# Kernel tuning notes

Measured on AMD Instinct MI355X. Metric: run time of the kernel, lower is better.

The kernel has to match this reference:

```python
import jax, jax.numpy as jnp
import numpy as np

DIM = 1024
HEADS = 16
D_HEAD = 64
INNER = HEADS * D_HEAD  # 1024
CTX_DIM = 768
FF_INNER = 4 * DIM  # 4096
EPS = 1e-5
SCALE = D_HEAD ** -0.5


def _layer_norm(x, g, b):
    m = jnp.mean(x, axis=-1, keepdims=True)
    v = jnp.mean(jnp.square(x - m), axis=-1, keepdims=True)
    return (x - m) * jax.lax.rsqrt(v + EPS) * g + b


def _attention(x, ctx, wq, wk, wv, wo, bo):
    B, S, _ = x.shape
    T = ctx.shape[1]
    # project and split heads -> [B, H, S, Dh]
    q = (x @ wq).reshape(B, S, HEADS, D_HEAD).transpose(0, 2, 1, 3)
    k = (ctx @ wk).reshape(B, T, HEADS, D_HEAD).transpose(0, 2, 1, 3)
    v = (ctx @ wv).reshape(B, T, HEADS, D_HEAD).transpose(0, 2, 1, 3)
    attn = jnp.einsum('bhid,bhjd->bhij', q, k) * SCALE
    attn = jax.nn.softmax(attn, axis=-1)
    out = jnp.einsum('bhij,bhjd->bhid', attn, v)  # [B, H, S, Dh]
    out = out.transpose(0, 2, 1, 3).reshape(B, S, INNER)
    return out @ wo + bo


def setup_inputs() -> dict:
    key = jax.random.key(0)
    ks = jax.random.split(key, 20)
    rn = lambda k, shape, s=0.02: jax.random.normal(k, shape, dtype=jnp.float32) * s
    inp = {
        'hidden_states': jax.random.normal(ks[0], (4, 2048, DIM), dtype=jnp.float32),
        'context': jax.random.normal(ks[1], (4, 77, CTX_DIM), dtype=jnp.float32),
        # self-attention
        'wq1': rn(ks[2], (DIM, INNER)), 'wk1': rn(ks[3], (DIM, INNER)),
        'wv1': rn(ks[4], (DIM, INNER)),
        'wo1': rn(ks[5], (INNER, DIM)), 'bo1': jnp.zeros((DIM,), jnp.float32),
        # cross-attention (k/v from context dim 768)
        'wq2': rn(ks[6], (DIM, INNER)), 'wk2': rn(ks[7], (CTX_DIM, INNER)),
        'wv2': rn(ks[8], (CTX_DIM, INNER)),
        'wo2': rn(ks[9], (INNER, DIM)), 'bo2': jnp.zeros((DIM,), jnp.float32),
        # GEGLU feed-forward
        'w_ff1': rn(ks[10], (DIM, 2 * FF_INNER)), 'b_ff1': jnp.zeros((2 * FF_INNER,), jnp.float32),
        'w_ff2': rn(ks[11], (FF_INNER, DIM)), 'b_ff2': jnp.zeros((DIM,), jnp.float32),
        # layer norms
        'ln1_g': jnp.ones((DIM,), jnp.float32), 'ln1_b': jnp.zeros((DIM,), jnp.float32),
        'ln2_g': jnp.ones((DIM,), jnp.float32), 'ln2_b': jnp.zeros((DIM,), jnp.float32),
        'ln3_g': jnp.ones((DIM,), jnp.float32), 'ln3_b': jnp.zeros((DIM,), jnp.float32),
    }
    return inp


def reference(hidden_states, context, wq1, wk1, wv1, wo1, bo1,
              wq2, wk2, wv2, wo2, bo2, w_ff1, b_ff1, w_ff2, b_ff2,
              ln1_g, ln1_b, ln2_g, ln2_b, ln3_g, ln3_b):
    # self-attention, pre-norm residual
    h = hidden_states
    h = h + _attention(_layer_norm(h, ln1_g, ln1_b), _layer_norm(h, ln1_g, ln1_b),
                       wq1, wk1, wv1, wo1, bo1)
    # cross-attention
    h = h + _attention(_layer_norm(h, ln2_g, ln2_b), context,
                       wq2, wk2, wv2, wo2, bo2)
    # GEGLU feed-forward
    x = _layer_norm(h, ln3_g, ln3_b) @ w_ff1 + b_ff1
    lin, gate = jnp.split(x, 2, axis=2)
    h = h + (lin * jax.nn.gelu(gate)) @ w_ff2 + b_ff2
    return h
```

## Files before the change

kernel.cpp:

```cpp
#include <hip/hip_runtime.h>

#define DIMM 1024
#define NHEADS 16
#define DHEAD 64
#define BATCH 4
#define SEQ 2048
#define TCTX 77
#define CTXD 768
#define FFI 4096

typedef float f32x4 __attribute__((ext_vector_type(4)));
typedef __bf16 bf16x8 __attribute__((ext_vector_type(8)));

__device__ __forceinline__ float bf2f(unsigned short u){
  union { unsigned int i; float f; } c; c.i = ((unsigned int)u) << 16; return c.f;
}
__device__ __forceinline__ unsigned short f2bf(float f){
  union { float f; unsigned int i; } c; c.f = f;
  unsigned int i = c.i;
  return (unsigned short)((i + 0x7fffu + ((i >> 16) & 1u)) >> 16);
}
__device__ __forceinline__ unsigned short f2bf_fast(float f){
  union { float f; unsigned int i; } c; c.f = f;
  return (unsigned short)((c.i + 0x8000u) >> 16);
}
__device__ __forceinline__ void cp16(const unsigned short* g, unsigned short* l){
  __builtin_amdgcn_global_load_lds(
      (const __attribute__((address_space(1))) unsigned int*)g,
      (__attribute__((address_space(3))) unsigned int*)l, 16, 0, 0);
}

__global__ __launch_bounds__(256) void ln_kernel(const float* __restrict__ x,
                                                 const float* __restrict__ g,
                                                 const float* __restrict__ bb,
                                                 unsigned short* __restrict__ y)
{
  int row = blockIdx.x, tid = threadIdx.x;
  float4 raw = ((const float4*)(x + (size_t)row * DIMM))[tid];
  float v0 = raw.x, v1 = raw.y, v2 = raw.z, v3 = raw.w;
  float s  = v0 + v1 + v2 + v3;
  float sq = v0*v0 + v1*v1 + v2*v2 + v3*v3;
  #pragma unroll
  for (int off = 32; off; off >>= 1){ s += __shfl_xor(s, off); sq += __shfl_xor(sq, off); }
  __shared__ float sm[8];
  int wave = tid >> 6, lane = tid & 63;
  if (lane == 0){ sm[wave] = s; sm[4 + wave] = sq; }
  __syncthreads();
  s  = sm[0] + sm[1] + sm[2] + sm[3];
  sq = sm[4] + sm[5] + sm[6] + sm[7];
  float mean = s * (1.f / DIMM);
  float var  = sq * (1.f / DIMM) - mean * mean;
  float rstd = rsqrtf(var + 1e-5f);
  float4 gr = ((const float4*)g)[tid];
  float4 br = ((const float4*)bb)[tid];
  ushort4 o;
  o.x = f2bf((v0 - mean) * rstd * gr.x + br.x);
  o.y = f2bf((v1 - mean) * rstd * gr.y + br.y);
  o.z = f2bf((v2 - mean) * rstd * gr.z + br.z);
  o.w = f2bf((v3 - mean) * rstd * gr.w + br.w);
  ((ushort4*)(y + (size_t)row * DIMM))[tid] = o;
}

__global__ __launch_bounds__(256) void wt_kernel(const float* __restrict__ in,
                                                 unsigned short* __restrict__ out,
                                                 int K, int N)
{
  __shared__ float t[32][33];
  int tx = threadIdx.x & 31, ty = threadIdx.x >> 5;
  int k0 = blockIdx.y * 32, n0 = blockIdx.x * 32;
  #pragma unroll
  for (int i = 0; i < 4; i++)
    t[ty + i * 8][tx] = in[(size_t)(k0 + ty + i * 8) * N + n0 + tx];
  __syncthreads();
  #pragma unroll
  for (int i = 0; i < 4; i++)
    out[(size_t)(n0 + ty + i * 8) * K + k0 + tx] = f2bf(t[tx][ty + i * 8]);
}

#define CTXE (TCTX * BATCH * CTXD)
__global__ __launch_bounds__(256) void ctxcvt_kernel(const float* __restrict__ in,
                                                     unsigned short* __restrict__ out)
{
  int e = (blockIdx.x * 256 + threadIdx.x) * 4;
  float4 v;
  if (e < CTXE) v = *(const float4*)(in + e);
  else { v.x = 0.f; v.y = 0.f; v.z = 0.f; v.w = 0.f; }
  ushort4 o; o.x = f2bf(v.x); o.y = f2bf(v.y); o.z = f2bf(v.z); o.w = f2bf(v.w);
  *(ushort4*)(out + e) = o;
}

template<int RESF, int CF32>
__global__ __launch_bounds__(256) void gemm_bt(
    const unsigned short* __restrict__ A, int lda,
    const unsigned short* __restrict__ Bt, int ldb,
    const float* __restrict__ bias, const void* __restrict__ resv,
    void* __restrict__ Cv, int ldc,
    int M, int N, int K)
{
  __shared__ __align__(16) unsigned short As[128][64];
  __shared__ __align__(16) unsigned short Bs[128][64];
  int tid = threadIdx.x;
  int n0 = blockIdx.x * 128, row0 = blockIdx.y * 128;
  int wave = tid >> 6, lane = tid & 63, quad = lane >> 4, l16 = lane & 15;
  int wm = (wave >> 1) * 64, wn = (wave & 1) * 64;
  int wrow = wave * 32;
  int lrow = lane >> 3, lgrp = lane & 7;
  int gcol = ((lgrp ^ lrow) * 8);

  f32x4 acc[4][4];
  #pragma unroll
  for (int mt = 0; mt < 4; mt++)
    #pragma unroll
    for (int nt = 0; nt < 4; nt++) acc[mt][nt] = 0.f;

  for (int k0 = 0; k0 < K; k0 += 64) {
    const unsigned short* ga = A  + (size_t)(row0 + wrow + lrow) * lda + k0 + gcol;
    const unsigned short* gb = Bt + (size_t)(n0  + wrow + lrow) * ldb + k0 + gcol;
    #pragma unroll
    for (int i = 0; i < 4; i++){
      cp16(ga + (size_t)(8 * i) * lda, &As[wrow + 8 * i][0]);
      cp16(gb + (size_t)(8 * i) * ldb, &Bs[wrow + 8 * i][0]);
    }
    __syncthreads();
    #pragma unroll
    for (int kc = 0; kc < 2; kc++){
      bf16x8 af[4], bf[4];
      #pragma unroll
      for (int mt = 0; mt < 4; mt++){
        int R = wm + mt * 16 + l16;
        af[mt] = *(const bf16x8*)&As[R][((kc * 4 + quad) ^ (R & 7)) * 8];
      }
      #pragma unroll
      for (int nt = 0; nt < 4; nt++){
        int R = wn + nt * 16 + l16;
        bf[nt] = *(const bf16x8*)&Bs[R][((kc * 4 + quad) ^ (R & 7)) * 8];
      }
      #pragma unroll
      for (int mt = 0; mt < 4; mt++)
        #pragma unroll
        for (int nt = 0; nt < 4; nt++)
          acc[mt][nt] = __builtin_amdgcn_mfma_f32_16x16x32_bf16(af[mt], bf[nt], acc[mt][nt], 0, 0, 0);
    }
    __syncthreads();
  }

  #pragma unroll
  for (int nt = 0; nt < 4; nt++){
    int c = n0 + wn + nt * 16 + l16;
    float bv = bias ? bias[c] : 0.f;
    #pragma unroll
    for (int mt = 0; mt < 4; mt++){
      int rbase = row0 + wm + mt * 16 + quad * 4;
      #pragma unroll
      for (int rr = 0; rr < 4; rr++){
        int r = rbase + rr;
        if (r < M) {
          float val = acc[mt][nt][rr] + bv;
          size_t idx = (size_t)r * ldc + c;
          if (RESF) val += ((const float*)resv)[idx];
          if (CF32) ((float*)Cv)[idx] = val;
          else      ((unsigned short*)Cv)[idx] = f2bf(val);
        }
      }
    }
  }
}

__global__ __launch_bounds__(256) void ff1_geglu_bt(
    const unsigned short* __restrict__ A,
    const unsigned short* __restrict__ BtW,
    const float* __restrict__ bias,
    unsigned short* __restrict__ Z, int M)
{
  __shared__ __align__(16) unsigned short As[128][64];
  __shared__ __align__(16) unsigned short BsL[128][64];
  __shared__ __align__(16) unsigned short BsG[128][64];
  int tid = threadIdx.x;
  int n0 = blockIdx.x * 128, row0 = blockIdx.y * 128;
  int wave = tid >> 6, lane = tid & 63, quad = lane >> 4, l16 = lane & 15;
  int wm = (wave >> 1) * 64, wn = (wave & 1) * 64;
  int wrow = wave * 32;
  int lrow = lane >> 3, lgrp = lane & 7;
  int gcol = ((lgrp ^ lrow) * 8);

  f32x4 accL[4][4], accG[4][4];
  #pragma unroll
  for (int mt = 0; mt < 4; mt++)
    #pragma unroll
    for (int nt = 0; nt < 4; nt++){ accL[mt][nt] = 0.f; accG[mt][nt] = 0.f; }

  for (int k0 = 0; k0 < DIMM; k0 += 64) {
    const unsigned short* ga = A   + (size_t)(row0 + wrow + lrow) * DIMM + k0 + gcol;
    const unsigned short* gl = BtW + (size_t)(n0  + wrow + lrow) * DIMM + k0 + gcol;
    const unsigned short* gg = BtW + (size_t)(FFI + n0 + wrow + lrow) * DIMM + k0 + gcol;
    #pragma unroll
    for (int i = 0; i < 4; i++){
      cp16(ga + (size_t)(8 * i) * DIMM, &As[wrow + 8 * i][0]);
      cp16(gl + (size_t)(8 * i) * DIMM, &BsL[wrow + 8 * i][0]);
      cp16(gg + (size_t)(8 * i) * DIMM, &BsG[wrow + 8 * i][0]);
    }
    __syncthreads();
    #pragma unroll
    for (int kc = 0; kc < 2; kc++){
      bf16x8 af[4], b[4];
      #pragma unroll
      for (int mt = 0; mt < 4; mt++){
        int R = wm + mt * 16 + l16;
        af[mt] = *(const bf16x8*)&As[R][((kc * 4 + quad) ^ (R & 7)) * 8];
      }
      #pragma unroll
      for (int nt = 0; nt < 4; nt++){
        int R = wn + nt * 16 + l16;
        b[nt] = *(const bf16x8*)&BsL[R][((kc * 4 + quad) ^ (R & 7)) * 8];
      }
      #pragma unroll
      for (int mt = 0; mt < 4; mt++)
        #pragma unroll
        for (int nt = 0; nt < 4; nt++)
          accL[mt][nt] = __builtin_amdgcn_mfma_f32_16x16x32_bf16(af[mt], b[nt], accL[mt][nt], 0, 0, 0);
      #pragma unroll
      for (int nt = 0; nt < 4; nt++){
        int R = wn + nt * 16 + l16;
        b[nt] = *(const bf16x8*)&BsG[R][((kc * 4 + quad) ^ (R & 7)) * 8];
      }
      #pragma unroll
      for (int mt = 0; mt < 4; mt++)
        #pragma unroll
        for (int nt = 0; nt < 4; nt++)
          accG[mt][nt] = __builtin_amdgcn_mfma_f32_16x16x32_bf16(af[mt], b[nt], accG[mt][nt], 0, 0, 0);
    }
    __syncthreads();
  }

  #pragma unroll
  for (int nt = 0; nt < 4; nt++){
    int c = n0 + wn + nt * 16 + l16;
    float bvL = bias[c];
    float bvG = bias[c + FFI];
    #pragma unroll
    for (int mt = 0; mt < 4; mt++){
      int rbase = row0 + wm + mt * 16 + quad * 4;
      #pragma unroll
      for (int rr = 0; rr < 4; rr++){
        float lin = accL[mt][nt][rr] + bvL;
        float g   = accG[mt][nt][rr] + bvG;
        float t = tanhf(0.7978845608028654f * (g + 0.044715f * g * g * g));
        Z[(size_t)(rbase + rr) * FFI + c] = f2bf(lin * 0.5f * g * (1.f + t));
      }
    }
  }
}

__global__ __launch_bounds__(256) void attn_mfma(
    const unsigned short* __restrict__ Q, int ldq,
    const unsigned short* __restrict__ Kb,
    const unsigned short* __restrict__ Vb, int ldkv,
    unsigned short* __restrict__ O,
    int S, int T, float scale)
{
  int tid = threadIdx.x, wave = tid >> 6, lane = tid & 63;
  int quad = lane >> 4, l16 = lane & 15;
  int bh = blockIdx.y, b = bh >> 4, h = bh & 15;
  int qw = blockIdx.x * 128 + wave * 32;

  __shared__ __align__(16) unsigned short Ks[64][72];
  __shared__ __align__(16) unsigned short Vt[64][72];
  __shared__ __align__(16) unsigned short Ps[4][32][72];

  bf16x8 Qf[2][2];
  #pragma unroll
  for (int mt = 0; mt < 2; mt++)
    #pragma unroll
    for (int kc = 0; kc < 2; kc++){
      const unsigned short* qp = Q + ((size_t)b * S + qw + mt * 16 + l16) * ldq
                                   + h * DHEAD + kc * 32 + quad * 8;
      union { float4 v; unsigned short u[8]; } ld; ld.v = *(const float4*)qp;
      union { bf16x8 v; unsigned short u[8]; } sc;
      #pragma unroll
      for (int j = 0; j < 8; j++) sc.u[j] = f2bf(bf2f(ld.u[j]) * scale);
      Qf[mt][kc] = sc.v;
    }

  f32x4 Oacc[2][4];
  float lp[2][4];
  #pragma unroll
  for (int mt = 0; mt < 2; mt++){
    #pragma unroll
    for (int nt = 0; nt < 4; nt++) Oacc[mt][nt] = 0.f;
    #pragma unroll
    for (int rr = 0; rr < 4; rr++) lp[mt][rr] = 0.f;
  }

  for (int j0 = 0; j0 < T; j0 += 64){
    #pragma unroll
    for (int p = 0; p < 2; p++){
      int key = p * 32 + (tid >> 3);
      int d0 = (tid & 7) * 8;
      union { float4 v; unsigned short u[8]; } kv;
      if (j0 + key < T) kv.v = *(const float4*)(Kb + ((size_t)b * T + j0 + key) * ldkv + h * DHEAD + d0);
      else { kv.v.x = 0.f; kv.v.y = 0.f; kv.v.z = 0.f; kv.v.w = 0.f; }
      *(float4*)&Ks[key][d0] = kv.v;
    }
    {
      int j = tid & 63, dbs = (tid >> 6) * 16;
      if (j0 + j < T){
        union { float4 v; unsigned short u[8]; } v1, v2;
        const unsigned short* vp = Vb + ((size_t)b * T + j0 + j) * ldkv + h * DHEAD + dbs;
        v1.v = ((const float4*)vp)[0];
        v2.v = ((const float4*)vp)[1];
        #pragma unroll
        for (int u = 0; u < 8; u++){ Vt[dbs + u][j] = v1.u[u]; Vt[dbs + 8 + u][j] = v2.u[u]; }
      } else {
        #pragma unroll
        for (int u = 0; u < 8; u++){ Vt[dbs + u][j] = 0; Vt[dbs + 8 + u][j] = 0; }
      }
    }
    __syncthreads();

    bool tail = (j0 + 64 > T);

    #pragma unroll
    for (int mt = 0; mt < 2; mt++){
      f32x4 s[4];
      #pragma unroll
      for (int nt = 0; nt < 4; nt++){
        s[nt] = 0.f;
        #pragma unroll
        for (int kc = 0; kc < 2; kc++){
          bf16x8 kf = *(const bf16x8*)&Ks[nt * 16 + l16][kc * 32 + quad * 8];
          s[nt] = __builtin_amdgcn_mfma_f32_16x16x32_bf16(Qf[mt][kc], kf, s[nt], 0, 0, 0);
        }
      }
      if (tail){
        #pragma unroll
        for (int nt = 0; nt < 4; nt++){
          bool valid = (j0 + nt * 16 + l16) < T;
          #pragma unroll
          for (int rr = 0; rr < 4; rr++) s[nt][rr] = valid ? s[nt][rr] : -1e30f;
        }
      }
      #pragma unroll
      for (int nt = 0; nt < 4; nt++)
        #pragma unroll
        for (int rr = 0; rr < 4; rr++){
          float p = __expf(fminf(s[nt][rr], 75.f));
          lp[mt][rr] += p;
          Ps[wave][mt * 16 + quad * 4 + rr][nt * 16 + l16] = f2bf_fast(p);
        }
    }

    #pragma unroll
    for (int kc = 0; kc < 2; kc++){
      bf16x8 pf[2];
      #pragma unroll
      for (int mt = 0; mt < 2; mt++)
        pf[mt] = *(const bf16x8*)&Ps[wave][mt * 16 + l16][kc * 32 + quad * 8];
      #pragma unroll
      for (int nt = 0; nt < 4; nt++){
        bf16x8 vf = *(const bf16x8*)&Vt[nt * 16 + l16][kc * 32 + quad * 8];
        #pragma unroll
        for (int mt = 0; mt < 2; mt++)
          Oacc[mt][nt] = __builtin_amdgcn_mfma_f32_16x16x32_bf16(pf[mt], vf, Oacc[mt][nt], 0, 0, 0);
      }
    }
    __syncthreads();
  }

  #pragma unroll
  for (int mt = 0; mt < 2; mt++){
    float inv[4];
    #pragma unroll
    for (int rr = 0; rr < 4; rr++){
      float l = lp[mt][rr];
      #pragma unroll
      for (int off = 1; off < 16; off <<= 1) l += __shfl_xor(l, off);
      inv[rr] = 1.f / l;
    }
    #pragma unroll
    for (int nt = 0; nt < 4; nt++)
      #pragma unroll
      for (int rr = 0; rr < 4; rr++){
        size_t idx = ((size_t)b * S + qw + mt * 16 + quad * 4 + rr) * DIMM
                     + h * DHEAD + nt * 16 + l16;
        O[idx] = f2bf(Oacc[mt][nt][rr] * inv[rr]);
      }
  }
}

extern "C" void kernel_launch(void* const* d_in, const int* in_sizes, int n_in,
                              void* d_out, int out_size, void* d_ws, size_t ws_size,
                              hipStream_t stream)
{
  const float* h0   = (const float*)d_in[0];
  const float* ctx  = (const float*)d_in[1];
  const float* wq1  = (const float*)d_in[2];
  const float* wk1  = (const float*)d_in[3];
  const float* wv1  = (const float*)d_in[4];
  const float* wo1  = (const float*)d_in[5];
  const float* bo1  = (const float*)d_in[6];
  const float* wq2  = (const float*)d_in[7];
  const float* wk2  = (const float*)d_in[8];
  const float* wv2  = (const float*)d_in[9];
  const float* wo2  = (const float*)d_in[10];
  const float* bo2  = (const float*)d_in[11];
  const float* wff1 = (const float*)d_in[12];
  const float* bff1 = (const float*)d_in[13];
  const float* wff2 = (const float*)d_in[14];
  const float* bff2 = (const float*)d_in[15];
  const float* ln1g = (const float*)d_in[16];
  const float* ln1b = (const float*)d_in[17];
  const float* ln2g = (const float*)d_in[18];
  const float* ln2b = (const float*)d_in[19];
  const float* ln3g = (const float*)d_in[20];
  const float* ln3b = (const float*)d_in[21];

  unsigned short* wsp = (unsigned short*)d_ws;
  const size_t RD = (size_t)BATCH * SEQ * DIMM;
  unsigned short* xn  = wsp;
  unsigned short* qkv = wsp + RD;
  unsigned short* ar  = wsp + 4 * RD;
  unsigned short* zb  = qkv;
  float* hres = (float*)d_out;

  const size_t M1 = (size_t)1024 * 1024;
  const int ROWS = BATCH * SEQ;
  const int CROWS = BATCH * TCTX;
  const float scale = 0.125f;
  dim3 blk(256);
  dim3 attn_grid(SEQ / 128, BATCH * NHEADS);

  wt_kernel<<<dim3(32, 32), blk, 0, stream>>>(wq1, ar,          DIMM, DIMM);
  wt_kernel<<<dim3(32, 32), blk, 0, stream>>>(wk1, ar + M1,     DIMM, DIMM);
  wt_kernel<<<dim3(32, 32), blk, 0, stream>>>(wv1, ar + 2 * M1, DIMM, DIMM);
  wt_kernel<<<dim3(32, 32), blk, 0, stream>>>(wo1, ar + 3 * M1, DIMM, DIMM);
  ln_kernel<<<ROWS, blk, 0, stream>>>(h0, ln1g, ln1b, xn);
  gemm_bt<0,0><<<dim3(3072 / 128, ROWS / 128), blk, 0, stream>>>(
      xn, DIMM, ar, DIMM, nullptr, nullptr, qkv, 3072, ROWS, 3072, DIMM);
  attn_mfma<<<attn_grid, blk, 0, stream>>>(qkv, 3072, qkv + 1024, qkv + 2048, 3072, xn, SEQ, SEQ, scale);
  gemm_bt<1,1><<<dim3(DIMM / 128, ROWS / 128), blk, 0, stream>>>(
      xn, DIMM, ar + 3 * M1, DIMM, bo1, h0, hres, DIMM, ROWS, DIMM, DIMM);

  unsigned short* wq2T  = ar;
  unsigned short* wkv2T = ar + M1;
  unsigned short* wo2T  = ar + M1 + (size_t)2048 * CTXD;
  unsigned short* xc    = wo2T + M1;
  wt_kernel<<<dim3(32, 32), blk, 0, stream>>>(wq2, wq2T, DIMM, DIMM);
  wt_kernel<<<dim3(32, 24), blk, 0, stream>>>(wk2, wkv2T, CTXD, DIMM);
  wt_kernel<<<dim3(32, 24), blk, 0, stream>>>(wv2, wkv2T + (size_t)1024 * CTXD, CTXD, DIMM);
  wt_kernel<<<dim3(32, 32), blk, 0, stream>>>(wo2, wo2T, DIMM, DIMM);
  ctxcvt_kernel<<<(384 * CTXD / 4) / 256, blk, 0, stream>>>(ctx, xc);
  ln_kernel<<<ROWS, blk, 0, stream>>>(hres, ln2g, ln2b, xn);
  gemm_bt<0,0><<<dim3(DIMM / 128, ROWS / 128), blk, 0, stream>>>(
      xn, DIMM, wq2T, DIMM, nullptr, nullptr, qkv, DIMM, ROWS, DIMM, DIMM);
  unsigned short* kvc = qkv + RD;
  gemm_bt<0,0><<<dim3(2048 / 128, 3), blk, 0, stream>>>(
      xc, CTXD, wkv2T, CTXD, nullptr, nullptr, kvc, 2048, CROWS, 2048, CTXD);
  attn_mfma<<<attn_grid, blk, 0, stream>>>(qkv, 1024, kvc, kvc + 1024, 2048, xn, SEQ, TCTX, scale);
  gemm_bt<1,1><<<dim3(DIMM / 128, ROWS / 128), blk, 0, stream>>>(
      xn, DIMM, wo2T, DIMM, bo2, hres, hres, DIMM, ROWS, DIMM, DIMM);

  unsigned short* wff1T = ar;
  unsigned short* wff2T = ar + 8 * M1;
  wt_kernel<<<dim3(256, 32),  blk, 0, stream>>>(wff1, wff1T, DIMM, 2 * FFI);
  wt_kernel<<<dim3(32, 128),  blk, 0, stream>>>(wff2, wff2T, FFI, DIMM);
  ln_kernel<<<ROWS, blk, 0, stream>>>(hres, ln3g, ln3b, xn);
  for (int half = 0; half < 2; half++){
    int r0 = half * 4096;
    ff1_geglu_bt<<<dim3(FFI / 128, 4096 / 128), blk, 0, stream>>>(
        xn + (size_t)r0 * DIMM, wff1T, bff1, zb, 4096);
    gemm_bt<1,1><<<dim3(DIMM / 128, 4096 / 128), blk, 0, stream>>>(
        zb, FFI, wff2T, FFI, bff2, hres + (size_t)r0 * DIMM,
        hres + (size_t)r0 * DIMM, DIMM, 4096, DIMM, FFI);
  }
}
```

Baseline: 1.101 ms.

## Keep attention probabilities in registers via transposed QK MFMA; use exp2 softmax

The attention kernel now computes the transposed score tile (K as the A operand), so each lane's score outputs already sit in the layout the PV MFMA needs as its A operand. The probabilities are packed straight into registers instead of going through the shared-memory Ps buffer, which removes those LDS writes and reads. The V fragment reads from LDS are rearranged to match the new key ordering. The softmax now uses exp2 with log2(e) folded into the Q scale, and the row-sum reduction is simplified. The GEGLU epilogue swaps tanhf for an exp2/rcp formulation, which is cheaper but slightly less accurate.

Result: faster. 1.016 ms (-7.8%).

```diff
diff --git a/kernel.cpp b/kernel.cpp
--- a/kernel.cpp
+++ b/kernel.cpp
@@ -19,10 +19,6 @@
   union { float f; unsigned int i; } c; c.f = f;
   unsigned int i = c.i;
   return (unsigned short)((i + 0x7fffu + ((i >> 16) & 1u)) >> 16);
-}
-__device__ __forceinline__ unsigned short f2bf_fast(float f){
-  union { float f; unsigned int i; } c; c.f = f;
-  return (unsigned short)((c.i + 0x8000u) >> 16);
 }
 __device__ __forceinline__ void cp16(const unsigned short* g, unsigned short* l){
   __builtin_amdgcn_global_load_lds(
@@ -244,7 +240,9 @@
       for (int rr = 0; rr < 4; rr++){
         float lin = accL[mt][nt][rr] + bvL;
         float g   = accG[mt][nt][rr] + bvG;
-        float t = tanhf(0.7978845608028654f * (g + 0.044715f * g * g * g));
+        float y = 0.7978845608028654f * (g + 0.044715f * g * g * g);
+        float e = __builtin_amdgcn_exp2f(y * 2.8853900817779268f);
+        float t = 1.f - 2.f * __builtin_amdgcn_rcpf(e + 1.f);
         Z[(size_t)(rbase + rr) * FFI + c] = f2bf(lin * 0.5f * g * (1.f + t));
       }
     }
@@ -265,8 +263,8 @@
 
   __shared__ __align__(16) unsigned short Ks[64][72];
   __shared__ __align__(16) unsigned short Vt[64][72];
-  __shared__ __align__(16) unsigned short Ps[4][32][72];
-
+
+  float qs = scale * 1.44269504088896f;
   bf16x8 Qf[2][2];
   #pragma unroll
   for (int mt = 0; mt < 2; mt++)
@@ -277,29 +275,26 @@
       union { float4 v; unsigned short u[8]; } ld; ld.v = *(const float4*)qp;
       union { bf16x8 v; unsigned short u[8]; } sc;
       #pragma unroll
-      for (int j = 0; j < 8; j++) sc.u[j] = f2bf(bf2f(ld.u[j]) * scale);
+      for (int j = 0; j < 8; j++) sc.u[j] = f2bf(bf2f(ld.u[j]) * qs);
       Qf[mt][kc] = sc.v;
     }
 
   f32x4 Oacc[2][4];
-  float lp[2][4];
-  #pragma unroll
-  for (int mt = 0; mt < 2; mt++){
+  float lp[2] = {0.f, 0.f};
+  #pragma unroll
+  for (int mt = 0; mt < 2; mt++)
     #pragma unroll
     for (int nt = 0; nt < 4; nt++) Oacc[mt][nt] = 0.f;
-    #pragma unroll
-    for (int rr = 0; rr < 4; rr++) lp[mt][rr] = 0.f;
-  }
 
   for (int j0 = 0; j0 < T; j0 += 64){
     #pragma unroll
     for (int p = 0; p < 2; p++){
       int key = p * 32 + (tid >> 3);
       int d0 = (tid & 7) * 8;
-      union { float4 v; unsigned short u[8]; } kv;
-      if (j0 + key < T) kv.v = *(const float4*)(Kb + ((size_t)b * T + j0 + key) * ldkv + h * DHEAD + d0);
-      else { kv.v.x = 0.f; kv.v.y = 0.f; kv.v.z = 0.f; kv.v.w = 0.f; }
-      *(float4*)&Ks[key][d0] = kv.v;
+      float4 kv;
+      if (j0 + key < T) kv = *(const float4*)(Kb + ((size_t)b * T + j0 + key) * ldkv + h * DHEAD + d0);
+      else { kv.x = 0.f; kv.y = 0.f; kv.z = 0.f; kv.w = 0.f; }
+      *(float4*)&Ks[key][d0] = kv;
     }
     {
       int j = tid & 63, dbs = (tid >> 6) * 16;
@@ -319,63 +314,55 @@
 
     bool tail = (j0 + 64 > T);
 
+    union pfu { bf16x8 v; __bf16 e[8]; } pf[2][2];
+
     #pragma unroll
     for (int mt = 0; mt < 2; mt++){
-      f32x4 s[4];
+      f32x4 sT[4];
       #pragma unroll
       for (int nt = 0; nt < 4; nt++){
-        s[nt] = 0.f;
+        sT[nt] = 0.f;
         #pragma unroll
         for (int kc = 0; kc < 2; kc++){
           bf16x8 kf = *(const bf16x8*)&Ks[nt * 16 + l16][kc * 32 + quad * 8];
-          s[nt] = __builtin_amdgcn_mfma_f32_16x16x32_bf16(Qf[mt][kc], kf, s[nt], 0, 0, 0);
+          sT[nt] = __builtin_amdgcn_mfma_f32_16x16x32_bf16(kf, Qf[mt][kc], sT[nt], 0, 0, 0);
         }
       }
-      if (tail){
-        #pragma unroll
-        for (int nt = 0; nt < 4; nt++){
-          bool valid = (j0 + nt * 16 + l16) < T;
-          #pragma unroll
-          for (int rr = 0; rr < 4; rr++) s[nt][rr] = valid ? s[nt][rr] : -1e30f;
+      #pragma unroll
+      for (int nt = 0; nt < 4; nt++)
+        #pragma unroll
+        for (int rr = 0; rr < 4; rr++){
+          float sv = sT[nt][rr];
+          if (tail && (j0 + nt * 16 + quad * 4 + rr) >= T) sv = -1e30f;
+          float p = __builtin_amdgcn_exp2f(fminf(sv, 108.f));
+          lp[mt] += p;
+          pf[mt][nt >> 1].e[(nt & 1) * 4 + rr] = (__bf16)p;
         }
-      }
-      #pragma unroll
-      for (int nt = 0; nt < 4; nt++)
-        #pragma unroll
-        for (int rr = 0; rr < 4; rr++){
-          float p = __expf(fminf(s[nt][rr], 75.f));
-          lp[mt][rr] += p;
-          Ps[wave][mt * 16 + quad * 4 + rr][nt * 16 + l16] = f2bf_fast(p);
-        }
-    }
-
-    #pragma unroll
-    for (int kc = 0; kc < 2; kc++){
-      bf16x8 pf[2];
-      #pragma unroll
-      for (int mt = 0; mt < 2; mt++)
-        pf[mt] = *(const bf16x8*)&Ps[wave][mt * 16 + l16][kc * 32 + quad * 8];
+    }
+
+    #pragma unroll
+    for (int kc = 0; kc < 2; kc++)
       #pragma unroll
       for (int nt = 0; nt < 4; nt++){
-        bf16x8 vf = *(const bf16x8*)&Vt[nt * 16 + l16][kc * 32 + quad * 8];
+        union { bf16x8 v; ushort4 u[2]; } vf;
+        vf.u[0] = *(const ushort4*)&Vt[nt * 16 + l16][kc * 32 + quad * 4];
+        vf.u[1] = *(const ushort4*)&Vt[nt * 16 + l16][kc * 32 + 16 + quad * 4];
         #pragma unroll
         for (int mt = 0; mt < 2; mt++)
-          Oacc[mt][nt] = __builtin_amdgcn_mfma_f32_16x16x32_bf16(pf[mt], vf, Oacc[mt][nt], 0, 0, 0);
-      }
-    }
+          Oacc[mt][nt] = __builtin_amdgcn_mfma_f32_16x16x32_bf16(pf[mt][kc].v, vf.v, Oacc[mt][nt], 0, 0, 0);
+      }
     __syncthreads();
   }
 
   #pragma unroll
   for (int mt = 0; mt < 2; mt++){
+    float l = lp[mt];
+    l += __shfl_xor(l, 16);
+    l += __shfl_xor(l, 32);
     float inv[4];
     #pragma unroll
-    for (int rr = 0; rr < 4; rr++){
-      float l = lp[mt][rr];
-      #pragma unroll
-      for (int off = 1; off < 16; off <<= 1) l += __shfl_xor(l, off);
-      inv[rr] = 1.f / l;
-    }
+    for (int rr = 0; rr < 4; rr++)
+      inv[rr] = 1.f / __shfl(l, quad * 4 + rr);
     #pragma unroll
     for (int nt = 0; nt < 4; nt++)
       #pragma unroll
```
